# Performance work log

Measured on AMD Instinct MI355X. Metric: run time of the kernel, lower is better.

## Reference

```python
import jax, jax.numpy as jnp
import numpy as np

N = 131072       # total nodes (B graphs x P nodes)
P = 4096         # nodes per graph
B = 32           # graphs in batch
E = 2097152      # edges (avg degree 16)
IN_DIM = 64
HID = 128
OUT = 16
EPS = 1e-5
SLOPE = 0.01


def _degrees(idx):
    # structural degree, clamped to min 1 (as DGL GraphConv does)
    d = jax.ops.segment_sum(jnp.ones((E,), jnp.float32), idx, num_segments=N)
    return jnp.maximum(d, 1.0)


def _graph_conv(x, W, src, dst, ew):
    # DGL GraphConv, norm='both', bias=False, with scalar edge weights:
    # h = D_out^{-1/2} x ; m_v = sum_{(u->v)} w_e h_u ; out = (D_in^{-1/2} m) W
    h = x * jax.lax.rsqrt(_degrees(src))[:, None]
    m = jax.ops.segment_sum(ew[:, None] * h[src], dst, num_segments=N)  # [N, F]
    return (m * jax.lax.rsqrt(_degrees(dst))[:, None]) @ W


def _graph_norm(x, gamma, beta, alpha):
    # GraphNorm (Cai et al. / PyG, batch=None): stats over all nodes per feature
    mu = jnp.mean(x, axis=0)
    c = x - alpha * mu
    var = jnp.mean(c * c, axis=0)
    return c * jax.lax.rsqrt(var + EPS) * gamma + beta


def _mean_nodes(h, gid):
    # per-graph mean readout; every graph has exactly P nodes
    return jax.ops.segment_sum(h, gid, num_segments=B) / P


def setup_inputs() -> dict:
    key = jax.random.key(0)
    ks = jax.random.split(key, 8)
    src = jax.random.randint(ks[0], (E,), 0, N, dtype=jnp.int32)
    # keep edges within each 4096-node graph block (batched DGL graph)
    dst = (src // P) * P + jax.random.randint(ks[1], (E,), 0, P, dtype=jnp.int32)
    features = jax.random.normal(ks[2], (N, IN_DIM), jnp.float32)
    edge_weights = jax.random.uniform(ks[3], (E,), jnp.float32)
    # kaiming/xavier-scale init approximations
    W1 = jax.random.normal(ks[4], (IN_DIM, HID), jnp.float32) * np.sqrt(2.0 / IN_DIM)
    W2 = jax.random.normal(ks[5], (HID, HID), jnp.float32) * np.sqrt(2.0 / HID)
    Wc = jax.random.normal(ks[6], (OUT, 2 * HID), jnp.float32) * np.sqrt(1.0 / (2 * HID))
    ones = jnp.ones((HID,), jnp.float32)
    zeros = jnp.zeros((HID,), jnp.float32)
    return {
        'features': features, 'edge_weights': edge_weights, 'src': src, 'dst': dst,
        'W1': W1, 'W2': W2, 'Wc': Wc,
        'gamma1': ones, 'beta1': zeros, 'alpha1': ones,
        'gamma2': ones, 'beta2': zeros, 'alpha2': ones,
    }


def reference(features, edge_weights, src, dst, W1, W2, Wc,
              gamma1, beta1, alpha1, gamma2, beta2, alpha2):
    gid = jnp.arange(N, dtype=jnp.int32) // P  # node -> graph id
    h1 = _graph_conv(features, W1, src, dst, edge_weights)
    h1 = jax.nn.leaky_relu(_graph_norm(h1, gamma1, beta1, alpha1), SLOPE)
    r1 = _mean_nodes(h1, gid)                  # [B, HID]
    h2 = _graph_conv(h1, W2, src, dst, edge_weights)
    h2 = jax.nn.leaky_relu(_graph_norm(h2, gamma2, beta2, alpha2), SLOPE)
    r2 = _mean_nodes(h2, gid)                  # [B, HID]
    readouts = jnp.concatenate([r1, r2], axis=1)  # [B, 2*HID]
    return readouts @ Wc.T                     # [B, OUT]
```

## Files before the change

kernel.cpp:

```cpp
#include <hip/hip_runtime.h>
#include <hip/hip_fp16.h>

constexpr int NN   = 131072;
constexpr int PP   = 4096;
constexpr int BG   = 32;
constexpr int EE   = 2097152;
constexpr int IND  = 64;
constexpr int HH   = 128;
constexpr int CAP  = 81920;
constexpr float EPSV   = 1e-5f;
constexpr float SLOPEV = 0.01f;

typedef short bf16x8 __attribute__((ext_vector_type(8)));
typedef float f32x4  __attribute__((ext_vector_type(4)));
typedef float f32x2  __attribute__((ext_vector_type(2)));

__device__ __forceinline__ unsigned f2bf(float f) {
    unsigned u = __float_as_uint(f);
    return (u + 0x7FFFu + ((u >> 16) & 1u)) >> 16;
}
__device__ __forceinline__ unsigned pack2bf(float lo, float hi) {
    return f2bf(lo) | (f2bf(hi) << 16);
}
__device__ __forceinline__ float bflo(unsigned p) { return __uint_as_float(p << 16); }
__device__ __forceinline__ float bfhi(unsigned p) { return __uint_as_float(p & 0xFFFF0000u); }
__device__ __forceinline__ float w16(unsigned r) {
    return __half2float(__ushort_as_half((unsigned short)(r >> 16)));
}
__device__ __forceinline__ void acc8(float& a0, float& a1, float& a2, float& a3,
                                     float& a4, float& a5, float& a6, float& a7,
                                     uint2 q, unsigned rec) {
    float w = w16(rec);
    f32x2 l0 = __builtin_amdgcn_cvt_pk_f32_fp8((int)q.x, false);
    f32x2 h0 = __builtin_amdgcn_cvt_pk_f32_fp8((int)q.x, true);
    f32x2 l1 = __builtin_amdgcn_cvt_pk_f32_fp8((int)q.y, false);
    f32x2 h1 = __builtin_amdgcn_cvt_pk_f32_fp8((int)q.y, true);
    a0 += w * l0.x; a1 += w * l0.y; a2 += w * h0.x; a3 += w * h0.y;
    a4 += w * l1.x; a5 += w * l1.y; a6 += w * h1.x; a7 += w * h1.y;
}

template <int K>
__device__ __forceinline__ void packw_body(const float* __restrict__ W,
                                           unsigned short* __restrict__ pw, int t) {
    if (t >= K * 16) return;
    int lane = t & 63, nt = (t >> 6) & 7, kt = t >> 9;
    int kbase = kt * 32 + ((lane >> 4) & 3) * 8;
    int col   = nt * 16 + (lane & 15);
    for (int j = 0; j < 8; j++)
        pw[t * 8 + j] = (unsigned short)f2bf(W[(kbase + j) * HH + col]);
}

__global__ __launch_bounds__(256) void k_prep(const float* __restrict__ features,
                                              unsigned* __restrict__ f8x,
                                              const float* __restrict__ W1,
                                              unsigned short* __restrict__ pw1,
                                              const float* __restrict__ W2,
                                              unsigned short* __restrict__ pw2,
                                              int* __restrict__ gcur,
                                              float* __restrict__ racc,
                                              unsigned* __restrict__ csr2) {
    int b = blockIdx.x, t = threadIdx.x;
    if (b < 8192) {
        int i = b * 256 + t;
        float4 v = ((const float4*)features)[i];
        int w0 = __builtin_amdgcn_cvt_pk_fp8_f32(v.x, v.y, 0, false);
        int w1 = __builtin_amdgcn_cvt_pk_fp8_f32(v.z, v.w, w0, true);
        f8x[i] = (unsigned)w1;
        return;
    }
    if (b == 8192) {
        if (t < BG) gcur[t * 16] = t * CAP;
        for (int i = t; i < 2 * BG * HH; i += 256) racc[i] = 0.f;
        return;
    }
    if (b < 8197) { packw_body<64>(W1, pw1, (b - 8193) * 256 + t); return; }
    if (b < 8205) { packw_body<128>(W2, pw2, (b - 8197) * 256 + t); return; }
    ((uint4*)csr2)[(b - 8205) * 256 + t] = make_uint4(0, 0, 0, 0);
}

__global__ __launch_bounds__(256) void k_part(const int* __restrict__ src,
                                              const int* __restrict__ dst,
                                              const float* __restrict__ ew,
                                              int* __restrict__ gcur,
                                              uint2* __restrict__ recs) {
    __shared__ int cnt[32];
    __shared__ int start[32];
    __shared__ int gbase[32];
    __shared__ uint2 stage[4096];
    int t = threadIdx.x;
    int ebase = blockIdx.x * 4096;
    if (t < 32) cnt[t] = 0;
    __syncthreads();
    int es[16]; int ed[16]; float ev[16];
#pragma unroll
    for (int k = 0; k < 16; k++) {
        int e = ebase + k * 256 + t;
        es[k] = src[e]; ed[k] = dst[e]; ev[k] = ew[e];
        atomicAdd(&cnt[es[k] >> 12], 1);
    }
    __syncthreads();
    if (t == 0) {
        int run = 0;
        for (int g = 0; g < 32; g++) { start[g] = run; run += cnt[g]; }
    }
    __syncthreads();
    if (t < 32) {
        gbase[t] = atomicAdd(&gcur[t * 16], cnt[t]);
        cnt[t] = start[t];
    }
    __syncthreads();
#pragma unroll
    for (int k = 0; k < 16; k++) {
        int g = es[k] >> 12;
        int pos = atomicAdd(&cnt[g], 1);
        stage[pos] = make_uint2((unsigned)(es[k] & 4095) | ((unsigned)(ed[k] & 4095) << 12) |
                                ((unsigned)g << 24), __float_as_uint(ev[k]));
    }
    __syncthreads();
    for (int i = t; i < 4096; i += 256) {
        uint2 r = stage[i];
        int g = r.x >> 24;
        recs[gbase[g] + (i - start[g])] = r;
    }
}

__global__ __launch_bounds__(1024) void k_hist(const uint2* __restrict__ recs,
                                               const int* __restrict__ gcur,
                                               int* __restrict__ shist,
                                               int* __restrict__ dhist) {
    __shared__ int hs[4096];
    __shared__ int hd[4096];
    int t = threadIdx.x;
    int g = blockIdx.x >> 3, c = blockIdx.x & 7;
    int n = gcur[g * 16] - g * CAP;
    int lo = (n * c) >> 3, hi = (n * (c + 1)) >> 3;
    ((int4*)hs)[t] = make_int4(0, 0, 0, 0);
    ((int4*)hd)[t] = make_int4(0, 0, 0, 0);
    __syncthreads();
    const uint2* base = recs + (size_t)g * CAP;
    for (int i = lo + t; i < hi; i += 1024) {
        unsigned x = base[i].x;
        atomicAdd(&hs[x & 4095], 1);
        atomicAdd(&hd[(x >> 12) & 4095], 1);
    }
    __syncthreads();
    ((int4*)(shist + (size_t)blockIdx.x * 4096))[t] = ((int4*)hs)[t];
    ((int4*)(dhist + (size_t)blockIdx.x * 4096))[t] = ((int4*)hd)[t];
}

__global__ __launch_bounds__(1024) void k_offs(int* __restrict__ shist,
                                               int* __restrict__ dhist,
                                               float* __restrict__ rs_s,
                                               float* __restrict__ rsd,
                                               int* __restrict__ degd,
                                               int* __restrict__ offs) {
    __shared__ int partial[1024];
    int t = threadIdx.x, g = blockIdx.x;
    int sdeg[4] = {0, 0, 0, 0}, ddeg[4] = {0, 0, 0, 0};
#pragma unroll
    for (int c = 0; c < 8; c++) {
        int4 sv = ((const int4*)(shist + (size_t)(g * 8 + c) * 4096))[t];
        int4 dv = ((const int4*)(dhist + (size_t)(g * 8 + c) * 4096))[t];
        sdeg[0] += sv.x; sdeg[1] += sv.y; sdeg[2] += sv.z; sdeg[3] += sv.w;
        ddeg[0] += dv.x; ddeg[1] += dv.y; ddeg[2] += dv.z; ddeg[3] += dv.w;
    }
    int pdeg[4];
#pragma unroll
    for (int j = 0; j < 4; j++) {
        int idx = t * 4 + j;
        int vs = sdeg[j]; if (vs < 1) vs = 1;
        rs_s[g * PP + idx] = rsqrtf((float)vs);
        int vd = ddeg[j]; if (vd < 1) vd = 1;
        rsd[g * PP + idx]  = rsqrtf((float)vd);
        pdeg[j] = (ddeg[j] + 3) & ~3;
        degd[g * PP + idx] = pdeg[j];
    }
    partial[t] = pdeg[0] + pdeg[1] + pdeg[2] + pdeg[3];
    __syncthreads();
    for (int off = 1; off < 1024; off <<= 1) {
        int v = partial[t];
        int add = (t >= off) ? partial[t - off] : 0;
        __syncthreads();
        partial[t] = v + add;
        __syncthreads();
    }
    int run = (t == 0) ? 0 : partial[t - 1];
#pragma unroll
    for (int j = 0; j < 4; j++) {
        int idx = t * 4 + j;
        offs[g * PP + idx] = g * CAP + run;
        int nb = run;
        for (int c = 0; c < 8; c++) {
            size_t hidx = (size_t)(g * 8 + c) * 4096 + idx;
            int v = dhist[hidx];
            dhist[hidx] = nb;
            nb += v;
        }
        run += pdeg[j];
    }
}

__global__ __launch_bounds__(1024) void k_place(const uint2* __restrict__ recs,
                                                const int* __restrict__ gcur,
                                                const int* __restrict__ dhist,
                                                const float* __restrict__ rs_s,
                                                unsigned* __restrict__ csr2) {
    __shared__ int cur[4096];
    __shared__ float rss[4096];
    int t = threadIdx.x;
    int g = blockIdx.x >> 3, c = blockIdx.x & 7;
    int n = gcur[g * 16] - g * CAP;
    int lo = (n * c) >> 3, hi = (n * (c + 1)) >> 3;
    ((int4*)cur)[t] = ((const int4*)(dhist + (size_t)blockIdx.x * 4096))[t];
    ((float4*)rss)[t] = ((const float4*)(rs_s + (size_t)g * PP))[t];
    __syncthreads();
    const uint2* base = recs + (size_t)g * CAP;
    unsigned* cbase = csr2 + (size_t)g * CAP;
    for (int i = lo + t; i < hi; i += 1024) {
        uint2 r = base[i];
        int sl = r.x & 4095, dl = (r.x >> 12) & 4095;
        int pos = atomicAdd(&cur[dl], 1);
        float wf = __uint_as_float(r.y) * rss[sl];
        cbase[pos] = (unsigned)sl | ((unsigned)__half_as_ushort(__float2half(wf)) << 16);
    }
}

__global__ __launch_bounds__(256) void k_aggemm1(const unsigned* __restrict__ f8x,
                                                 const unsigned* __restrict__ csr2,
                                                 const int* __restrict__ offs,
                                                 const int* __restrict__ degd,
                                                 const float* __restrict__ rsd,
                                                 const short* __restrict__ PW,
                                                 unsigned short* __restrict__ C,
                                                 float* __restrict__ part) {
    constexpr int WP = 36;
    __shared__ unsigned lds[64 * WP];
    __shared__ float s1[HH], s2[HH];
    int t = threadIdx.x;
    if (t < HH) { s1[t] = 0.f; s2[t] = 0.f; }
    int bid = blockIdx.x;
    int xcd = bid & 7, idx = bid >> 3;
    int g = xcd * 4 + (idx >> 6);
    int node0 = g * PP + (idx & 63) * 64;
    int lane = t & 63, wv = t >> 6;
    int eid = lane >> 3, ql = lane & 7;
    const uint2* hp8 = (const uint2*)(f8x + (size_t)((unsigned)(g * PP)) * 16) + ql;
    {
        int lrA = wv * 16 + eid * 2;
        int va = node0 + lrA, vb = va + 1;
        int oa = offs[va], ca = degd[va];
        int ob = offs[vb], cb = degd[vb];
        float A0=0.f,A1=0.f,A2=0.f,A3=0.f,A4=0.f,A5=0.f,A6=0.f,A7=0.f;
        float B0=0.f,B1=0.f,B2=0.f,B3=0.f,B4=0.f,B5=0.f,B6=0.f,B7=0.f;
        int c0 = ca < cb ? ca : cb;
        int cm = ca < cb ? cb : ca;
        int i = 0;
        for (; i < c0; i += 4) {
            uint4 ra = *(const uint4*)(csr2 + oa + i);
            uint4 rb = *(const uint4*)(csr2 + ob + i);
            uint2 ga0 = hp8[(ra.x & 4095) * 8];
            uint2 ga1 = hp8[(ra.y & 4095) * 8];
            uint2 ga2 = hp8[(ra.z & 4095) * 8];
            uint2 ga3 = hp8[(ra.w & 4095) * 8];
            uint2 gb0 = hp8[(rb.x & 4095) * 8];
            uint2 gb1 = hp8[(rb.y & 4095) * 8];
            uint2 gb2 = hp8[(rb.z & 4095) * 8];
            uint2 gb3 = hp8[(rb.w & 4095) * 8];
            acc8(A0,A1,A2,A3,A4,A5,A6,A7, ga0, ra.x);
            acc8(A0,A1,A2,A3,A4,A5,A6,A7, ga1, ra.y);
            acc8(A0,A1,A2,A3,A4,A5,A6,A7, ga2, ra.z);
            acc8(A0,A1,A2,A3,A4,A5,A6,A7, ga3, ra.w);
            acc8(B0,B1,B2,B3,B4,B5,B6,B7, gb0, rb.x);
            acc8(B0,B1,B2,B3,B4,B5,B6,B7, gb1, rb.y);
            acc8(B0,B1,B2,B3,B4,B5,B6,B7, gb2, rb.z);
            acc8(B0,B1,B2,B3,B4,B5,B6,B7, gb3, rb.w);
        }
        if (i < cm) {
            int ot = (ca > cb) ? oa : ob;
            float E0=0.f,E1=0.f,E2=0.f,E3=0.f,E4=0.f,E5=0.f,E6=0.f,E7=0.f;
            for (; i < cm; i += 4) {
                uint4 rr = *(const uint4*)(csr2 + ot + i);
                uint2 g0 = hp8[(rr.x & 4095) * 8];
                uint2 g1 = hp8[(rr.y & 4095) * 8];
                uint2 g2 = hp8[(rr.z & 4095) * 8];
                uint2 g3 = hp8[(rr.w & 4095) * 8];
                acc8(E0,E1,E2,E3,E4,E5,E6,E7, g0, rr.x);
                acc8(E0,E1,E2,E3,E4,E5,E6,E7, g1, rr.y);
                acc8(E0,E1,E2,E3,E4,E5,E6,E7, g2, rr.z);
                acc8(E0,E1,E2,E3,E4,E5,E6,E7, g3, rr.w);
            }
            if (ca > cb) { A0+=E0;A1+=E1;A2+=E2;A3+=E3;A4+=E4;A5+=E5;A6+=E6;A7+=E7; }
            else         { B0+=E0;B1+=E1;B2+=E2;B3+=E3;B4+=E4;B5+=E5;B6+=E6;B7+=E7; }
        }
        float rda = rsd[va], rdb = rsd[vb];
        *(uint4*)&lds[lrA * WP + ql * 4] =
            make_uint4(pack2bf(A0*rda, A1*rda), pack2bf(A2*rda, A3*rda),
                       pack2bf(A4*rda, A5*rda), pack2bf(A6*rda, A7*rda));
        *(uint4*)&lds[(lrA + 1) * WP + ql * 4] =
            make_uint4(pack2bf(B0*rdb, B1*rdb), pack2bf(B2*rdb, B3*rdb),
                       pack2bf(B4*rdb, B5*rdb), pack2bf(B6*rdb, B7*rdb));
    }
    __syncthreads();
    int m = lane & 15, quad = lane >> 4;
    bf16x8 a[2];
#pragma unroll
    for (int kt = 0; kt < 2; kt++)
        a[kt] = *(const bf16x8*)&lds[(wv * 16 + m) * WP + kt * 16 + quad * 4];
#pragma unroll
    for (int nt = 0; nt < 8; nt++) {
        f32x4 acc = {0.f, 0.f, 0.f, 0.f};
#pragma unroll
        for (int kt = 0; kt < 2; kt++) {
            bf16x8 b = *(const bf16x8*)(PW + ((size_t)(kt * 8 + nt) * 64 + lane) * 8);
            acc = __builtin_amdgcn_mfma_f32_16x16x32_bf16(a[kt], b, acc, 0, 0, 0);
        }
        int col = nt * 16 + m;
        int r0 = node0 + wv * 16 + quad * 4;
        float ps = 0.f, pq = 0.f;
#pragma unroll
        for (int r = 0; r < 4; r++) {
            C[(size_t)(r0 + r) * HH + col] = (unsigned short)f2bf(acc[r]);
            ps += acc[r]; pq += acc[r] * acc[r];
        }
        atomicAdd(&s1[col], ps);
        atomicAdd(&s2[col], pq);
    }
    __syncthreads();
    if (t < HH) {
        part[bid * 256 + t]      = s1[t];
        part[bid * 256 + HH + t] = s2[t];
    }
}

__global__ __launch_bounds__(256) void k_aggemm2(const unsigned* __restrict__ f8,
                                                 const unsigned* __restrict__ csr2,
                                                 const int* __restrict__ offs,
                                                 const int* __restrict__ degd,
                                                 const float* __restrict__ rsd,
                                                 const short* __restrict__ PW,
                                                 unsigned short* __restrict__ C,
                                                 float* __restrict__ part) {
    constexpr int WP = 68;
    __shared__ unsigned lds[64 * WP];
    __shared__ float s1[HH], s2[HH];
    int t = threadIdx.x;
    if (t < HH) { s1[t] = 0.f; s2[t] = 0.f; }
    int bid = blockIdx.x;
    int xcd = bid & 7, idx = bid >> 3;
    int g = xcd * 4 + (idx >> 6);
    int node0 = g * PP + (idx & 63) * 64;
    int lane = t & 63, wv = t >> 6;
    int quad = lane >> 4, ql = lane & 15;
    const uint2* hp8 = (const uint2*)(f8 + (size_t)((unsigned)(g * PP)) * 32) + ql;
    for (int p = 0; p < 2; p++) {
        int lrA = wv * 16 + p * 8 + quad * 2;
        int va = node0 + lrA, vb = va + 1;
        int oa = offs[va], ca = degd[va];
        int ob = offs[vb], cb = degd[vb];
        float A0=0.f,A1=0.f,A2=0.f,A3=0.f,A4=0.f,A5=0.f,A6=0.f,A7=0.f;
        float B0=0.f,B1=0.f,B2=0.f,B3=0.f,B4=0.f,B5=0.f,B6=0.f,B7=0.f;
        int c0 = ca < cb ? ca : cb;
        int cm = ca < cb ? cb : ca;
        int i = 0;
        for (; i < c0; i += 4) {
            uint4 ra = *(const uint4*)(csr2 + oa + i);
            uint4 rb = *(const uint4*)(csr2 + ob + i);
            uint2 ga0 = hp8[(ra.x & 4095) * 16];
            uint2 ga1 = hp8[(ra.y & 4095) * 16];
            uint2 ga2 = hp8[(ra.z & 4095) * 16];
            uint2 ga3 = hp8[(ra.w & 4095) * 16];
            uint2 gb0 = hp8[(rb.x & 4095) * 16];
            uint2 gb1 = hp8[(rb.y & 4095) * 16];
            uint2 gb2 = hp8[(rb.z & 4095) * 16];
            uint2 gb3 = hp8[(rb.w & 4095) * 16];
            acc8(A0,A1,A2,A3,A4,A5,A6,A7, ga0, ra.x);
            acc8(A0,A1,A2,A3,A4,A5,A6,A7, ga1, ra.y);
            acc8(A0,A1,A2,A3,A4,A5,A6,A7, ga2, ra.z);
            acc8(A0,A1,A2,A3,A4,A5,A6,A7, ga3, ra.w);
            acc8(B0,B1,B2,B3,B4,B5,B6,B7, gb0, rb.x);
            acc8(B0,B1,B2,B3,B4,B5,B6,B7, gb1, rb.y);
            acc8(B0,B1,B2,B3,B4,B5,B6,B7, gb2, rb.z);
            acc8(B0,B1,B2,B3,B4,B5,B6,B7, gb3, rb.w);
        }
        if (i < cm) {
            int ot = (ca > cb) ? oa : ob;
            float E0=0.f,E1=0.f,E2=0.f,E3=0.f,E4=0.f,E5=0.f,E6=0.f,E7=0.f;
            for (; i < cm; i += 4) {
                uint4 rr = *(const uint4*)(csr2 + ot + i);
                uint2 g0 = hp8[(rr.x & 4095) * 16];
                uint2 g1 = hp8[(rr.y & 4095) * 16];
                uint2 g2 = hp8[(rr.z & 4095) * 16];
                uint2 g3 = hp8[(rr.w & 4095) * 16];
                acc8(E0,E1,E2,E3,E4,E5,E6,E7, g0, rr.x);
                acc8(E0,E1,E2,E3,E4,E5,E6,E7, g1, rr.y);
                acc8(E0,E1,E2,E3,E4,E5,E6,E7, g2, rr.z);
                acc8(E0,E1,E2,E3,E4,E5,E6,E7, g3, rr.w);
            }
            if (ca > cb) { A0+=E0;A1+=E1;A2+=E2;A3+=E3;A4+=E4;A5+=E5;A6+=E6;A7+=E7; }
            else         { B0+=E0;B1+=E1;B2+=E2;B3+=E3;B4+=E4;B5+=E5;B6+=E6;B7+=E7; }
        }
        float rda = rsd[va], rdb = rsd[vb];
        *(uint4*)&lds[lrA * WP + ql * 4] =
            make_uint4(pack2bf(A0*rda, A1*rda), pack2bf(A2*rda, A3*rda),
                       pack2bf(A4*rda, A5*rda), pack2bf(A6*rda, A7*rda));
        *(uint4*)&lds[(lrA + 1) * WP + ql * 4] =
            make_uint4(pack2bf(B0*rdb, B1*rdb), pack2bf(B2*rdb, B3*rdb),
                       pack2bf(B4*rdb, B5*rdb), pack2bf(B6*rdb, B7*rdb));
    }
    __syncthreads();
    int m = lane & 15, quad2 = lane >> 4;
    bf16x8 a[4];
#pragma unroll
    for (int kt = 0; kt < 4; kt++)
        a[kt] = *(const bf16x8*)&lds[(wv * 16 + m) * WP + kt * 16 + quad2 * 4];
#pragma unroll
    for (int nt = 0; nt < 8; nt++) {
        f32x4 acc = {0.f, 0.f, 0.f, 0.f};
#pragma unroll
        for (int kt = 0; kt < 4; kt++) {
            bf16x8 b = *(const bf16x8*)(PW + ((size_t)(kt * 8 + nt) * 64 + lane) * 8);
            acc = __builtin_amdgcn_mfma_f32_16x16x32_bf16(a[kt], b, acc, 0, 0, 0);
        }
        int col = nt * 16 + m;
        int r0 = node0 + wv * 16 + quad2 * 4;
        float ps = 0.f, pq = 0.f;
#pragma unroll
        for (int r = 0; r < 4; r++) {
            C[(size_t)(r0 + r) * HH + col] = (unsigned short)f2bf(acc[r]);
            ps += acc[r]; pq += acc[r] * acc[r];
        }
        atomicAdd(&s1[col], ps);
        atomicAdd(&s2[col], pq);
    }
    __syncthreads();
    if (t < HH) {
        part[bid * 256 + t]      = s1[t];
        part[bid * 256 + HH + t] = s2[t];
    }
}

__global__ __launch_bounds__(256) void k_red(const float* __restrict__ part,
                                             float* __restrict__ pb) {
    int t = threadIdx.x, b = blockIdx.x;
    float s = 0.f;
    for (int r = 0; r < 32; r++) s += part[(size_t)(b * 32 + r) * 256 + t];
    pb[b * 256 + t] = s;
}

__global__ void k_coef(const float* __restrict__ pb, const float* __restrict__ gamma,
                       const float* __restrict__ beta, const float* __restrict__ alpha,
                       float* __restrict__ ab) {
    int t = threadIdx.x;
    float s = 0.f;
    for (int b = 0; b < 64; b++) s += pb[b * 256 + t];
    __shared__ float sh[256];
    sh[t] = s;
    __syncthreads();
    if (t < 128) {
        float mu = sh[t] * (1.f / NN);
        float e2 = sh[128 + t] * (1.f / NN);
        float al = alpha[t];
        float var = e2 - (2.f * al - al * al) * mu * mu;
        float a = rsqrtf(var + EPSV) * gamma[t];
        ab[t] = a;
        ab[HH + t] = beta[t] - al * mu * a;
    }
}

template <bool WRITE>
__global__ __launch_bounds__(256) void k_normro(const unsigned* __restrict__ h,
                                                const float* __restrict__ ab,
                                                float* __restrict__ racc,
                                                unsigned short* __restrict__ f8) {
    int fp = threadIdx.x & 63;
    int q  = threadIdx.x >> 6;
    int bid = blockIdx.x;
    int xcd = bid & 7, idx = bid >> 3;
    int g = xcd * 4 + (idx >> 6);
    int node0 = g * PP + (idx & 63) * 64;
    float a0 = ab[2 * fp], a1 = ab[2 * fp + 1];
    float b0 = ab[HH + 2 * fp], b1 = ab[HH + 2 * fp + 1];
    float s0 = 0.f, s1 = 0.f;
    for (int i = q; i < 64; i += 4) {
        size_t idx2 = (size_t)(node0 + i) * 64 + fp;
        unsigned v = h[idx2];
        float x0 = fmaf(a0, bflo(v), b0); x0 = x0 > 0.f ? x0 : SLOPEV * x0;
        float x1 = fmaf(a1, bfhi(v), b1); x1 = x1 > 0.f ? x1 : SLOPEV * x1;
        if (WRITE) f8[idx2] = (unsigned short)__builtin_amdgcn_cvt_pk_fp8_f32(x0, x1, 0, false);
        s0 += x0; s1 += x1;
    }
    __shared__ float sh[512];
    sh[threadIdx.x] = s0;
    sh[256 + threadIdx.x] = s1;
    __syncthreads();
    if (q == 0) {
        float t0 = s0 + sh[64 + fp] + sh[128 + fp] + sh[192 + fp];
        float t1 = s1 + sh[256 + 64 + fp] + sh[256 + 128 + fp] + sh[256 + 192 + fp];
        atomicAdd(&racc[g * HH + 2 * fp],     t0);
        atomicAdd(&racc[g * HH + 2 * fp + 1], t1);
    }
}

__global__ void k_final(const float* __restrict__ racc1, const float* __restrict__ racc2,
                        const float* __restrict__ Wc, float* __restrict__ out) {
    int t = threadIdx.x;
    int b = t >> 4, o = t & 15;
    float acc = 0.f;
    for (int f = 0; f < HH; f++) acc += racc1[b * HH + f] * Wc[o * (2 * HH) + f];
    for (int f = 0; f < HH; f++) acc += racc2[b * HH + f] * Wc[o * (2 * HH) + HH + f];
    out[t] = acc * (1.f / PP);
}

extern "C" void kernel_launch(void* const* d_in, const int* in_sizes, int n_in,
                              void* d_out, int out_size, void* d_ws, size_t ws_size,
                              hipStream_t stream) {
    const float* features = (const float*)d_in[0];
    const float* ew       = (const float*)d_in[1];
    const int*   src      = (const int*)d_in[2];
    const int*   dst      = (const int*)d_in[3];
    const float* W1       = (const float*)d_in[4];
    const float* W2       = (const float*)d_in[5];
    const float* Wc       = (const float*)d_in[6];
    const float* gamma1   = (const float*)d_in[7];
    const float* beta1    = (const float*)d_in[8];
    const float* alpha1   = (const float*)d_in[9];
    const float* gamma2   = (const float*)d_in[10];
    const float* beta2    = (const float*)d_in[11];
    const float* alpha2   = (const float*)d_in[12];
    float* out = (float*)d_out;

    char* w = (char*)d_ws;
    int*    gcur   = (int*)(w + 0);
    float*  racc1  = (float*)(w + (16u << 10));
    float*  racc2  = (float*)(w + (32u << 10));
    float*  ab1    = (float*)(w + (48u << 10));
    float*  ab2    = (float*)(w + (52u << 10));
    unsigned short* pw1 = (unsigned short*)(w + (64u << 10));
    unsigned short* pw2 = (unsigned short*)(w + (80u << 10));
    float*  pb     = (float*)(w + (128u << 10));
    float*  rs_s   = (float*)(w + (1024u << 10));
    float*  rsd    = (float*)(w + (1536u << 10));
    int*    degd   = (int*)(w + (2048u << 10));
    int*    offs   = (int*)(w + (2560u << 10));
    float*  part   = (float*)(w + (3u << 20));
    int*    shist  = (int*)(w + (5u << 20));
    int*    dhist  = (int*)(w + (9u << 20));
    unsigned* csr2 = (unsigned*)(w + (13u << 20));
    unsigned* mbuf = (unsigned*)(w + (23u << 20));
    unsigned* hbuf = (unsigned*)(w + (55u << 20));
    uint2*    recs = (uint2*)(w + (87u << 20));
    unsigned* f8x  = (unsigned*)(w + (107u << 20));
    unsigned* f8buf= (unsigned*)(w + (123u << 20));

    k_prep<<<10765, 256, 0, stream>>>(features, f8x, W1, pw1, W2, pw2, gcur, racc1, csr2);

    k_part<<<EE / 4096, 256, 0, stream>>>(src, dst, ew, gcur, recs);
    k_hist<<<BG * 8, 1024, 0, stream>>>(recs, gcur, shist, dhist);
    k_offs<<<BG, 1024, 0, stream>>>(shist, dhist, rs_s, rsd, degd, offs);
    k_place<<<BG * 8, 1024, 0, stream>>>(recs, gcur, dhist, rs_s, csr2);

    k_aggemm1<<<NN / 64, 256, 0, stream>>>(f8x, csr2, offs, degd, rsd,
                                           (const short*)pw1, (unsigned short*)hbuf, part);
    k_red<<<64, 256, 0, stream>>>(part, pb);
    k_coef<<<1, 256, 0, stream>>>(pb, gamma1, beta1, alpha1, ab1);
    k_normro<true><<<NN / 64, 256, 0, stream>>>(hbuf, ab1, racc1, (unsigned short*)f8buf);

    k_aggemm2<<<NN / 64, 256, 0, stream>>>(f8buf, csr2, offs, degd, rsd,
                                           (const short*)pw2, (unsigned short*)mbuf, part);
    k_red<<<64, 256, 0, stream>>>(part, pb);
    k_coef<<<1, 256, 0, stream>>>(pb, gamma2, beta2, alpha2, ab2);
    k_normro<false><<<NN / 64, 256, 0, stream>>>(mbuf, ab2, racc2, nullptr);

    k_final<<<1, 512, 0, stream>>>(racc1, racc2, Wc, out);
}
```

Measured before the change: 359.0 us.

## Narrow per-lane gather in aggemm1 and store layer-2 output as fp8

The first aggregation kernel now has each lane gather 4 bytes (4 fp8 features) with 16 lanes per node, and processes two node pairs per lane instead of one, trading wider loads for more parallel lanes per row. The second aggregate-GEMM writes its pre-norm output as fp8 instead of bf16, halving that intermediate's write and the later read in a new dedicated norm/readout kernel. This lowers memory traffic but adds fp8 quantization error before GraphNorm statistics are applied, which may hurt accuracy.

```diff
diff --git a/kernel.cpp b/kernel.cpp
--- a/kernel.cpp
+++ b/kernel.cpp
@@ -26,6 +26,13 @@
 __device__ __forceinline__ float bfhi(unsigned p) { return __uint_as_float(p & 0xFFFF0000u); }
 __device__ __forceinline__ float w16(unsigned r) {
     return __half2float(__ushort_as_half((unsigned short)(r >> 16)));
+}
+__device__ __forceinline__ void edge_acc(float& a0, float& a1, float& a2, float& a3,
+                                         unsigned q, unsigned rec) {
+    f32x2 lo = __builtin_amdgcn_cvt_pk_f32_fp8((int)q, false);
+    f32x2 hi = __builtin_amdgcn_cvt_pk_f32_fp8((int)q, true);
+    float w = w16(rec);
+    a0 += w * lo.x; a1 += w * lo.y; a2 += w * hi.x; a3 += w * hi.y;
 }
 __device__ __forceinline__ void acc8(float& a0, float& a1, float& a2, float& a3,
                                      float& a4, float& a5, float& a6, float& a7,
@@ -243,62 +250,60 @@
     int g = xcd * 4 + (idx >> 6);
     int node0 = g * PP + (idx & 63) * 64;
     int lane = t & 63, wv = t >> 6;
-    int eid = lane >> 3, ql = lane & 7;
-    const uint2* hp8 = (const uint2*)(f8x + (size_t)((unsigned)(g * PP)) * 16) + ql;
-    {
-        int lrA = wv * 16 + eid * 2;
+    int q = lane >> 4, ql = lane & 15;
+    const unsigned* hp8 = f8x + (size_t)((unsigned)(g * PP)) * 16 + ql;
+    for (int p = 0; p < 2; p++) {
+        int lrA = wv * 16 + p * 8 + q * 2;
         int va = node0 + lrA, vb = va + 1;
         int oa = offs[va], ca = degd[va];
         int ob = offs[vb], cb = degd[vb];
-        float A0=0.f,A1=0.f,A2=0.f,A3=0.f,A4=0.f,A5=0.f,A6=0.f,A7=0.f;
-        float B0=0.f,B1=0.f,B2=0.f,B3=0.f,B4=0.f,B5=0.f,B6=0.f,B7=0.f;
+        float A0 = 0.f, A1 = 0.f, A2 = 0.f, A3 = 0.f;
+        float B0 = 0.f, B1 = 0.f, B2 = 0.f, B3 = 0.f;
         int c0 = ca < cb ? ca : cb;
         int cm = ca < cb ? cb : ca;
         int i = 0;
         for (; i < c0; i += 4) {
             uint4 ra = *(const uint4*)(csr2 + oa + i);
             uint4 rb = *(const uint4*)(csr2 + ob + i);
-            uint2 ga0 = hp8[(ra.x & 4095) * 8];
-            uint2 ga1 = hp8[(ra.y & 4095) * 8];
-            uint2 ga2 = hp8[(ra.z & 4095) * 8];
-            uint2 ga3 = hp8[(ra.w & 4095) * 8];
-            uint2 gb0 = hp8[(rb.x & 4095) * 8];
-            uint2 gb1 = hp8[(rb.y & 4095) * 8];
-            uint2 gb2 = hp8[(rb.z & 4095) * 8];
-            uint2 gb3 = hp8[(rb.w & 4095) * 8];
-            acc8(A0,A1,A2,A3,A4,A5,A6,A7, ga0, ra.x);
-            acc8(A0,A1,A2,A3,A4,A5,A6,A7, ga1, ra.y);
-            acc8(A0,A1,A2,A3,A4,A5,A6,A7, ga2, ra.z);
-            acc8(A0,A1,A2,A3,A4,A5,A6,A7, ga3, ra.w);
-            acc8(B0,B1,B2,B3,B4,B5,B6,B7, gb0, rb.x);
-            acc8(B0,B1,B2,B3,B4,B5,B6,B7, gb1, rb.y);
-            acc8(B0,B1,B2,B3,B4,B5,B6,B7, gb2, rb.z);
-            acc8(B0,B1,B2,B3,B4,B5,B6,B7, gb3, rb.w);
+            unsigned qa0 = hp8[(ra.x & 4095) * 16];
+            unsigned qa1 = hp8[(ra.y & 4095) * 16];
+            unsigned qa2 = hp8[(ra.z & 4095) * 16];
+            unsigned qa3 = hp8[(ra.w & 4095) * 16];
+            unsigned qb0 = hp8[(rb.x & 4095) * 16];
+            unsigned qb1 = hp8[(rb.y & 4095) * 16];
+            unsigned qb2 = hp8[(rb.z & 4095) * 16];
+            unsigned qb3 = hp8[(rb.w & 4095) * 16];
+            edge_acc(A0, A1, A2, A3, qa0, ra.x);
+            edge_acc(A0, A1, A2, A3, qa1, ra.y);
+            edge_acc(A0, A1, A2, A3, qa2, ra.z);
+            edge_acc(A0, A1, A2, A3, qa3, ra.w);
+            edge_acc(B0, B1, B2, B3, qb0, rb.x);
+            edge_acc(B0, B1, B2, B3, qb1, rb.y);
+            edge_acc(B0, B1, B2, B3, qb2, rb.z);
+            edge_acc(B0, B1, B2, B3, qb3, rb.w);
         }
         if (i < cm) {
             int ot = (ca > cb) ? oa : ob;
-            float E0=0.f,E1=0.f,E2=0.f,E3=0.f,E4=0.f,E5=0.f,E6=0.f,E7=0.f;
+            float E0 = 0.f, E1 = 0.f, E2 = 0.f, E3 = 0.f;
             for (; i < cm; i += 4) {
                 uint4 rr = *(const uint4*)(csr2 + ot + i);
-                uint2 g0 = hp8[(rr.x & 4095) * 8];
-                uint2 g1 = hp8[(rr.y & 4095) * 8];
-                uint2 g2 = hp8[(rr.z & 4095) * 8];
-                uint2 g3 = hp8[(rr.w & 4095) * 8];
-                acc8(E0,E1,E2,E3,E4,E5,E6,E7, g0, rr.x);
-                acc8(E0,E1,E2,E3,E4,E5,E6,E7, g1, rr.y);
-                acc8(E0,E1,E2,E3,E4,E5,E6,E7, g2, rr.z);
-                acc8(E0,E1,E2,E3,E4,E5,E6,E7, g3, rr.w);
+                unsigned q0 = hp8[(rr.x & 4095) * 16];
+                unsigned q1 = hp8[(rr.y & 4095) * 16];
+                unsigned q2 = hp8[(rr.z & 4095) * 16];
+                unsigned q3 = hp8[(rr.w & 4095) * 16];
+                edge_acc(E0, E1, E2, E3, q0, rr.x);
+                edge_acc(E0, E1, E2, E3, q1, rr.y);
+                edge_acc(E0, E1, E2, E3, q2, rr.z);
+                edge_acc(E0, E1, E2, E3, q3, rr.w);
             }
-            if (ca > cb) { A0+=E0;A1+=E1;A2+=E2;A3+=E3;A4+=E4;A5+=E5;A6+=E6;A7+=E7; }
-            else         { B0+=E0;B1+=E1;B2+=E2;B3+=E3;B4+=E4;B5+=E5;B6+=E6;B7+=E7; }
+            if (ca > cb) { A0 += E0; A1 += E1; A2 += E2; A3 += E3; }
+            else         { B0 += E0; B1 += E1; B2 += E2; B3 += E3; }
         }
         float rda = rsd[va], rdb = rsd[vb];
-        *(uint4*)&lds[lrA * WP + ql * 4] =
-            make_uint4(pack2bf(A0*rda, A1*rda), pack2bf(A2*rda, A3*rda),
-                       pack2bf(A4*rda, A5*rda), pack2bf(A6*rda, A7*rda));
-        *(uint4*)&lds[(lrA + 1) * WP + ql * 4] =
-            make_uint4(pack2bf(B0*rdb, B1*rdb), pack2bf(B2*rdb, B3*rdb),
-                       pack2bf(B4*rdb, B5*rdb), pack2bf(B6*rdb, B7*rdb));
+        *(uint2*)&lds[lrA * WP + ql * 2] =
+            make_uint2(pack2bf(A0 * rda, A1 * rda), pack2bf(A2 * rda, A3 * rda));
+        *(uint2*)&lds[(lrA + 1) * WP + ql * 2] =
+            make_uint2(pack2bf(B0 * rdb, B1 * rdb), pack2bf(B2 * rdb, B3 * rdb));
     }
     __syncthreads();
     int m = lane & 15, quad = lane >> 4;
@@ -338,7 +343,7 @@
                                                  const int* __restrict__ degd,
                                                  const float* __restrict__ rsd,
                                                  const short* __restrict__ PW,
-                                                 unsigned short* __restrict__ C,
+                                                 unsigned char* __restrict__ C8,
                                                  float* __restrict__ part) {
     constexpr int WP = 68;
     __shared__ unsigned lds[64 * WP];
@@ -426,7 +431,8 @@
         float ps = 0.f, pq = 0.f;
 #pragma unroll
         for (int r = 0; r < 4; r++) {
-            C[(size_t)(r0 + r) * HH + col] = (unsigned short)f2bf(acc[r]);
+            C8[(size_t)(r0 + r) * HH + col] =
+                (unsigned char)__builtin_amdgcn_cvt_pk_fp8_f32(acc[r], acc[r], 0, false);
             ps += acc[r]; pq += acc[r] * acc[r];
         }
         atomicAdd(&s1[col], ps);
@@ -467,11 +473,10 @@
     }
 }
 
-template <bool WRITE>
-__global__ __launch_bounds__(256) void k_normro(const unsigned* __restrict__ h,
-                                                const float* __restrict__ ab,
-                                                float* __restrict__ racc,
-                                                unsigned short* __restrict__ f8) {
+__global__ __launch_bounds__(256) void k_normro1(const unsigned* __restrict__ h,
+                                                 const float* __restrict__ ab,
+                                                 float* __restrict__ racc,
+                                                 unsigned short* __restrict__ f8) {
     int fp = threadIdx.x & 63;
     int q  = threadIdx.x >> 6;
     int bid = blockIdx.x;
@@ -486,7 +491,39 @@
         unsigned v = h[idx2];
         float x0 = fmaf(a0, bflo(v), b0); x0 = x0 > 0.f ? x0 : SLOPEV * x0;
         float x1 = fmaf(a1, bfhi(v), b1); x1 = x1 > 0.f ? x1 : SLOPEV * x1;
-        if (WRITE) f8[idx2] = (unsigned short)__builtin_amdgcn_cvt_pk_fp8_f32(x0, x1, 0, false);
+        f8[idx2] = (unsigned short)__builtin_amdgcn_cvt_pk_fp8_f32(x0, x1, 0, false);
+        s0 += x0; s1 += x1;
+    }
+    __shared__ float sh[512];
+    sh[threadIdx.x] = s0;
+    sh[256 + threadIdx.x] = s1;
+    __syncthreads();
+    if (q == 0) {
+        float t0 = s0 + sh[64 + fp] + sh[128 + fp] + sh[192 + fp];
+        float t1 = s1 + sh[256 + 64 + fp] + sh[256 + 128 + fp] + sh[256 + 192 + fp];
+        atomicAdd(&racc[g * HH + 2 * fp],     t0);
+        atomicAdd(&racc[g * HH + 2 * fp + 1], t1);
+    }
+}
+
+__global__ __launch_bounds__(256) void k_normro2(const unsigned short* __restrict__ h8,
+                                                 const float* __restrict__ ab,
+                                                 float* __restrict__ racc) {
+    int fp = threadIdx.x & 63;
+    int q  = threadIdx.x >> 6;
+    int bid = blockIdx.x;
+    int xcd = bid & 7, idx = bid >> 3;
+    int g = xcd * 4 + (idx >> 6);
+    int node0 = g * PP + (idx & 63) * 64;
+    float a0 = ab[2 * fp], a1 = ab[2 * fp + 1];
+    float b0 = ab[HH + 2 * fp], b1 = ab[HH + 2 * fp + 1];
+    float s0 = 0.f, s1 = 0.f;
+    for (int i = q; i < 64; i += 4) {
+        size_t idx2 = (size_t)(node0 + i) * 64 + fp;
+        unsigned short v = h8[idx2];
+        f32x2 xy = __builtin_amdgcn_cvt_pk_f32_fp8((int)(unsigned)v, false);
+        float x0 = fmaf(a0, xy.x, b0); x0 = x0 > 0.f ? x0 : SLOPEV * x0;
+        float x1 = fmaf(a1, xy.y, b1); x1 = x1 > 0.f ? x1 : SLOPEV * x1;
         s0 += x0; s1 += x1;
     }
     __shared__ float sh[512];
@@ -546,7 +583,7 @@
     int*    shist  = (int*)(w + (5u << 20));
     int*    dhist  = (int*)(w + (9u << 20));
     unsigned* csr2 = (unsigned*)(w + (13u << 20));
-    unsigned* mbuf = (unsigned*)(w + (23u << 20));
+    unsigned char* c8buf = (unsigned char*)(w + (23u << 20));
     unsigned* hbuf = (unsigned*)(w + (55u << 20));
     uint2*    recs = (uint2*)(w + (87u << 20));
     unsigned* f8x  = (unsigned*)(w + (107u << 20));
@@ -563,13 +600,13 @@
                                            (const short*)pw1, (unsigned short*)hbuf, part);
     k_red<<<64, 256, 0, stream>>>(part, pb);
     k_coef<<<1, 256, 0, stream>>>(pb, gamma1, beta1, alpha1, ab1);
-    k_normro<true><<<NN / 64, 256, 0, stream>>>(hbuf, ab1, racc1, (unsigned short*)f8buf);
+    k_normro1<<<NN / 64, 256, 0, stream>>>(hbuf, ab1, racc1, (unsigned short*)f8buf);
 
     k_aggemm2<<<NN / 64, 256, 0, stream>>>(f8buf, csr2, offs, degd, rsd,
-                                           (const short*)pw2, (unsigned short*)mbuf, part);
+                                           (const short*)pw2, c8buf, part);
     k_red<<<64, 256, 0, stream>>>(part, pb);
     k_coef<<<1, 256, 0, stream>>>(pb, gamma2, beta2, alpha2, ab2);
-    k_normro<false><<<NN / 64, 256, 0, stream>>>(mbuf, ab2, racc2, nullptr);
+    k_normro2<<<NN / 64, 256, 0, stream>>>((const unsigned short*)c8buf, ab2, racc2);
 
     k_final<<<1, 512, 0, stream>>>(racc1, racc2, Wc, out);
 }
```

New measurement: 361.1 us. Within noise of the previous version (+0.6%).
